# Kernel optimization log

Hardware: AMD Instinct MI355X
Metric: run time of the kernel (lower is better)

The kernel has to match this reference:

```python
import jax, jax.numpy as jnp
import numpy as np

B, N, L, E = 8, 2000, 128, 2048  # batch, nodes, local_size+1, ff_hidden_dim
PENALTY = 10.0


def setup_inputs() -> dict:
    key = jax.random.key(0)
    ks = jax.random.split(key, 8)
    dist = jax.random.uniform(ks[0], (B, N, N), jnp.float32) + 1e-3  # positive distances
    theta = jax.random.normal(ks[1], (B, N, N), jnp.float32)
    ins_feature0 = jax.random.normal(ks[2], (B, N, 1), jnp.float32)
    ins_feature1 = jax.random.normal(ks[3], (B, N, 1), jnp.float32)
    d_in = 2 * L + 2
    W1 = jax.random.normal(ks[4], (d_in, E), jnp.float32) * 0.02
    b1 = jnp.zeros((E,), jnp.float32)
    W2 = jax.random.normal(ks[5], (E, L), jnp.float32) * 0.02
    b2 = jnp.zeros((L,), jnp.float32)
    return {"theta": theta, "dist": dist, "ins_feature0": ins_feature0,
            "ins_feature1": ins_feature1, "W1": W1, "b1": b1, "W2": W2, "b2": b2}


def reference(theta, dist, ins_feature0, ins_feature1, W1, b1, W2, b2):
    k = W2.shape[1]  # local_size (L)
    # smallest-k along last dim, sorted ascending (torch.topk largest=False)
    neg_vals, idx = jax.lax.top_k(-dist, k)          # [B,N,L]
    sorted_dist = -neg_vals
    sorted_dist = sorted_dist / jnp.max(sorted_dist, axis=-1, keepdims=True)
    sorted_theta = jnp.take_along_axis(theta, idx, axis=-1)  # [B,N,L]
    x_in = jnp.concatenate([sorted_dist, sorted_theta, ins_feature0, ins_feature1], axis=-1)  # [B,N,2L+2]
    edge_emb = x_in @ W1 + b1                        # [B,N,E] (no nonlinearity, as in source)
    out = edge_emb @ W2 + b2 - sorted_dist           # [B,N,L]
    b_, n_, _ = dist.shape
    bi = jnp.arange(b_)[:, None, None]
    ni = jnp.arange(n_)[None, :, None]
    out_mat = jnp.full(dist.shape, PENALTY, dist.dtype).at[bi, ni, idx].set(out)
    return out_mat
```

## Files before the change

### kernel.cpp

```cpp
#include <hip/hip_runtime.h>
#include <hip/hip_bf16.h>

#define BN 8
#define NN 2000
#define LL 128
#define EE 2048
#define DIN 258
#define KPAD 264
#define NROWS (BN*NN)
#define PENALTY_V 10.0f
#define CANDCAP 256
#define T0 0.092f
#define SPLITK 16
#define ECHUNK (EE/SPLITK)
#define RPB 4
#define NBINS 256
#define AWORDS 5568

__global__ __launch_bounds__(256) void kA1(const float* __restrict__ W1,
                                           const float* __restrict__ b1,
                                           const float* __restrict__ W2,
                                           float* __restrict__ part) {
    __shared__ float As2[8][64];
    const int t = threadIdx.x;
    const int j = t & 127;
    const int half = t >> 7;
    const int rg = blockIdx.x >> 4;
    const int ks = blockIdx.x & 15;
    const int k0 = rg * 8;
    const int ebase = ks * ECHUNK;
    float acc[4] = {0.f, 0.f, 0.f, 0.f};
    for (int ec = ebase; ec < ebase + ECHUNK; ec += 64) {
        #pragma unroll
        for (int q = 0; q < 2; ++q) {
            int linear = q * 256 + t;
            int r8 = linear >> 6;
            int e  = linear & 63;
            int k  = k0 + r8;
            float v;
            if (k < DIN)       v = W1[k * EE + ec + e];
            else if (k == DIN) v = b1[ec + e];
            else               v = 0.0f;
            As2[r8][e] = v;
        }
        __syncthreads();
        #pragma unroll 8
        for (int e = 0; e < 64; ++e) {
            float w = W2[(ec + e) * LL + j];
            #pragma unroll
            for (int rr = 0; rr < 4; ++rr)
                acc[rr] += As2[half * 4 + rr][e] * w;
        }
        __syncthreads();
    }
    #pragma unroll
    for (int rr = 0; rr < 4; ++rr) {
        int k = k0 + half * 4 + rr;
        part[(size_t)ks * (KPAD * LL) + k * LL + j] = acc[rr];
    }
}

__global__ __launch_bounds__(256) void kA2(const float* __restrict__ part,
                                           const float* __restrict__ b2,
                                           float* __restrict__ Wc,
                                           float* __restrict__ bc) {
    const int i = blockIdx.x * 256 + threadIdx.x;
    float s = 0.f;
    #pragma unroll
    for (int q = 0; q < SPLITK; ++q) s += part[(size_t)q * (KPAD * LL) + i];
    const int k = i >> 7;
    const int j = i & 127;
    if (k == DIN)      { bc[j] = s + b2[j]; Wc[i] = 0.f; }
    else if (k > DIN)  { Wc[i] = 0.f; }
    else               { Wc[i] = s; }
}

__global__ __launch_bounds__(256) void kZ(unsigned int* __restrict__ cursor) {
    int i = blockIdx.x * 256 + threadIdx.x;
    if (i < NROWS) cursor[i] = 0u;
}

__global__ __launch_bounds__(256) void kPA(const float* __restrict__ dist,
                                           unsigned long long* __restrict__ candg,
                                           unsigned int* __restrict__ cursor) {
    const int t = threadIdx.x;
    const int lane = t & 63;
    const int row = blockIdx.x;
    unsigned int v[8];
    unsigned int mask8 = 0u;
    int cnt_l = 0;
    if (t < 250) {
        const uint4* d4 = (const uint4*)(dist + (size_t)row * NN);
        uint4 a = d4[2 * t], b = d4[2 * t + 1];
        v[0] = a.x; v[1] = a.y; v[2] = a.z; v[3] = a.w;
        v[4] = b.x; v[5] = b.y; v[6] = b.z; v[7] = b.w;
        #pragma unroll
        for (int e = 0; e < 8; ++e)
            if (__uint_as_float(v[e]) <= T0) mask8 |= (1u << e);
        cnt_l = __builtin_popcount(mask8);
    }
    int inc = cnt_l;
    #pragma unroll
    for (int d = 1; d < 64; d <<= 1) {
        int o = __shfl_up(inc, d);
        if (lane >= d) inc += o;
    }
    const int excl = inc - cnt_l;
    unsigned int ret = 0u;
    if (lane == 63) ret = atomicAdd(&cursor[row], (unsigned int)inc);
    const unsigned int base = (unsigned int)__shfl((int)ret, 63);
    unsigned int off = base + (unsigned int)excl;
    #pragma unroll
    for (int e = 0; e < 8; ++e) {
        if ((mask8 >> e) & 1u) {
            if (off < (unsigned int)CANDCAP)
                candg[(size_t)row * CANDCAP + off] =
                    ((unsigned long long)v[e] << 32) | (unsigned int)(8 * t + e);
            ++off;
        }
    }
}

__global__ __launch_bounds__(256) void kPB(const float* __restrict__ dist,
                                           const float* __restrict__ theta,
                                           const float* __restrict__ f0,
                                           const float* __restrict__ f1,
                                           const unsigned long long* __restrict__ candg,
                                           const unsigned int* __restrict__ cursor,
                                           const float* __restrict__ Wc,
                                           const float* __restrict__ bc,
                                           float* __restrict__ out) {
    __shared__ __align__(16) unsigned int arena[AWORDS];
    const int t = threadIdx.x;
    const int lane = t & 63;
    const int w = t >> 6;
    const int row = blockIdx.x * RPB + w;

    float* xv = (float*)&arena[4000 + w * 264];
    int* oidx = (int*)&arena[5056 + w * 128];
    const unsigned int cnt = cursor[row];

    if (cnt >= (unsigned int)LL && cnt <= (unsigned int)CANDCAP) {
        unsigned long long* keys = (unsigned long long*)&arena[w * 1000];
        unsigned long long k0v, k1v, k2v, k3v;
        {
            const unsigned long long* cg = candg + (size_t)row * CANDCAP;
            k0v = (lane        < (int)cnt) ? cg[lane]        : ~0ULL;
            k1v = (lane + 64   < (int)cnt) ? cg[lane + 64]   : ~0ULL;
            k2v = (lane + 128  < (int)cnt) ? cg[lane + 128]  : ~0ULL;
            k3v = (lane + 192  < (int)cnt) ? cg[lane + 192]  : ~0ULL;
            keys[lane] = k0v; keys[lane + 64] = k1v;
            keys[lane + 128] = k2v; keys[lane + 192] = k3v;
        }
        float th0 = 0.f, th1 = 0.f, th2 = 0.f, th3 = 0.f;
        if (k0v != ~0ULL) th0 = theta[(size_t)row * NN + (unsigned int)k0v];
        if (k1v != ~0ULL) th1 = theta[(size_t)row * NN + (unsigned int)k1v];
        if (k2v != ~0ULL) th2 = theta[(size_t)row * NN + (unsigned int)k2v];
        if (k3v != ~0ULL) th3 = theta[(size_t)row * NN + (unsigned int)k3v];
        unsigned int r0 = 0, r1 = 0, r2 = 0, r3 = 0;
        for (unsigned int j = 0; j < cnt; ++j) {
            const unsigned long long kj = keys[j];
            r0 += (kj < k0v); r1 += (kj < k1v);
            r2 += (kj < k2v); r3 += (kj < k3v);
        }
        if (k0v != ~0ULL && r0 < (unsigned int)LL) {
            xv[r0] = __uint_as_float((unsigned int)(k0v >> 32));
            xv[LL + r0] = th0; oidx[r0] = (int)(unsigned int)k0v;
        }
        if (k1v != ~0ULL && r1 < (unsigned int)LL) {
            xv[r1] = __uint_as_float((unsigned int)(k1v >> 32));
            xv[LL + r1] = th1; oidx[r1] = (int)(unsigned int)k1v;
        }
        if (k2v != ~0ULL && r2 < (unsigned int)LL) {
            xv[r2] = __uint_as_float((unsigned int)(k2v >> 32));
            xv[LL + r2] = th2; oidx[r2] = (int)(unsigned int)k2v;
        }
        if (k3v != ~0ULL && r3 < (unsigned int)LL) {
            xv[r3] = __uint_as_float((unsigned int)(k3v >> 32));
            xv[LL + r3] = th3; oidx[r3] = (int)(unsigned int)k3v;
        }
    } else {
        unsigned int* hist = &arena[w * 1000];
        unsigned long long* cand = (unsigned long long*)&arena[w * 1000 + 256];
        {
            uint4 z4 = {0u, 0u, 0u, 0u};
            *(uint4*)&hist[lane * 4] = z4;
            unsigned long long f1v = ~0ULL;
            #pragma unroll
            for (int q = 0; q < CANDCAP / 64; ++q) cand[lane + q * 64] = f1v;
        }
        unsigned int v[32];
        const int nv = (lane < 52) ? 32 : 28;
        {
            const uint4* drow4 = (const uint4*)(dist + (size_t)row * NN);
            #pragma unroll
            for (int q = 0; q < 8; ++q) {
                int qi = q * 64 + lane;
                if (qi < NN / 4) {
                    uint4 a = drow4[qi];
                    v[4 * q] = a.x; v[4 * q + 1] = a.y;
                    v[4 * q + 2] = a.z; v[4 * q + 3] = a.w;
                }
            }
        }
        float T = T0;
        unsigned int qm = 0u;
        {
            unsigned int lmax = 0u;
            #pragma unroll
            for (int k = 0; k < 32; ++k) if (k < nv) lmax = max(lmax, v[k]);
            #pragma unroll
            for (int d = 1; d < 64; d <<= 1) lmax = max(lmax, (unsigned int)__shfl_xor((int)lmax, d));
            float lo = 0.0f, hi = __uint_as_float(lmax);
            if (cnt < (unsigned int)LL) lo = T; else hi = T;
            for (int it = 0; it < 32; ++it) {
                T = 0.5f * (lo + hi);
                unsigned int m = 0u;
                #pragma unroll
                for (int k = 0; k < 32; ++k)
                    if (k < nv && __uint_as_float(v[k]) <= T) m |= (1u << k);
                int c = __builtin_popcount(m);
                #pragma unroll
                for (int d = 1; d < 64; d <<= 1) c += __shfl_xor(c, d);
                qm = m;
                if (c >= LL && c <= CANDCAP) break;
                if (c < LL) lo = T; else hi = T;
            }
        }
        const float scale2 = (float)(NBINS - 1) / T;
        #pragma unroll
        for (int k = 0; k < 32; ++k) {
            if ((qm >> k) & 1u) {
                float f = __uint_as_float(v[k]);
                int b = (int)(f * scale2);
                b = b > NBINS - 1 ? NBINS - 1 : b;
                atomicAdd(&hist[b], 1u);
            }
        }
        {
            uint4* h4 = (uint4*)&hist[lane * 4];
            uint4 a0 = *h4;
            unsigned int c[4] = {a0.x, a0.y, a0.z, a0.w};
            unsigned int loc[4], run = 0;
            #pragma unroll
            for (int k = 0; k < 4; ++k) { loc[k] = run; run += c[k]; }
            unsigned int inc = run;
            #pragma unroll
            for (int d = 1; d < 64; d <<= 1) {
                unsigned int o = (unsigned int)__shfl_up((int)inc, d);
                if (lane >= d) inc += o;
            }
            const unsigned int excl = inc - run;
            uint4 s0 = {excl + loc[0], excl + loc[1], excl + loc[2], excl + loc[3]};
            *h4 = s0;
        }
        #pragma unroll
        for (int k = 0; k < 32; ++k) {
            if ((qm >> k) & 1u) {
                unsigned int bits = v[k];
                float f = __uint_as_float(bits);
                int b = (int)(f * scale2);
                b = b > NBINS - 1 ? NBINS - 1 : b;
                unsigned int old = atomicAdd(&hist[b], 0x10000u);
                unsigned int slot = (old & 0xFFFFu) + (old >> 16);
                unsigned int idx = (unsigned int)((k >> 2) * 256 + lane * 4 + (k & 3));
                if (slot < (unsigned int)CANDCAP)
                    cand[slot] = ((unsigned long long)bits << 32) | idx;
            }
        }
        {
            unsigned long long key_s[CANDCAP / 64];
            float th_s[CANDCAP / 64];
            #pragma unroll
            for (int s = 0; s < CANDCAP / 64; ++s) key_s[s] = cand[lane + s * 64];
            #pragma unroll
            for (int s = 0; s < CANDCAP / 64; ++s)
                if (key_s[s] != ~0ULL)
                    th_s[s] = theta[(size_t)row * NN + (unsigned int)key_s[s]];
            #pragma unroll
            for (int s = 0; s < CANDCAP / 64; ++s) {
                unsigned long long key = key_s[s];
                if (key != ~0ULL) {
                    unsigned int bits = (unsigned int)(key >> 32);
                    unsigned int idx  = (unsigned int)key;
                    float f = __uint_as_float(bits);
                    int b = (int)(f * scale2);
                    b = b > NBINS - 1 ? NBINS - 1 : b;
                    unsigned int word = hist[b];
                    unsigned int start = word & 0xFFFFu;
                    unsigned int end = start + (word >> 16);
                    if (end > (unsigned int)CANDCAP) end = (unsigned int)CANDCAP;
                    unsigned int r = start;
                    for (unsigned int j = start; j < end; ++j) r += (cand[j] < key);
                    if (r < (unsigned int)LL) {
                        xv[r] = f;
                        xv[LL + r] = th_s[s];
                        oidx[r] = (int)idx;
                    }
                }
            }
        }
    }

    {
        const float rdm = 1.0f / xv[LL - 1];
        xv[lane] *= rdm;
        xv[lane + 64] *= rdm;
        if (lane == 0) {
            xv[256] = f0[row];
            xv[257] = f1[row];
            #pragma unroll
            for (int z = DIN; z < KPAD; ++z) xv[z] = 0.0f;
        }
    }

    __syncthreads();

    const int j = t & 127;
    const int rp = t >> 7;
    const float* x0 = (const float*)&arena[4000 + (2 * rp) * 264];
    const float* x1 = (const float*)&arena[4000 + (2 * rp + 1) * 264];
    float acc0 = bc[j] - x0[j];
    float acc1 = bc[j] - x1[j];
    #pragma unroll 2
    for (int k = 0; k < KPAD; k += 8) {
        float w0 = Wc[(k + 0) * LL + j];
        float w1 = Wc[(k + 1) * LL + j];
        float w2 = Wc[(k + 2) * LL + j];
        float w3 = Wc[(k + 3) * LL + j];
        float w4 = Wc[(k + 4) * LL + j];
        float w5 = Wc[(k + 5) * LL + j];
        float w6 = Wc[(k + 6) * LL + j];
        float w7 = Wc[(k + 7) * LL + j];
        float4 xa0 = *(const float4*)&x0[k];
        float4 xa1 = *(const float4*)&x0[k + 4];
        float4 xb0 = *(const float4*)&x1[k];
        float4 xb1 = *(const float4*)&x1[k + 4];
        acc0 += xa0.x * w0; acc1 += xb0.x * w0;
        acc0 += xa0.y * w1; acc1 += xb0.y * w1;
        acc0 += xa0.z * w2; acc1 += xb0.z * w2;
        acc0 += xa0.w * w3; acc1 += xb0.w * w3;
        acc0 += xa1.x * w4; acc1 += xb1.x * w4;
        acc0 += xa1.y * w5; acc1 += xb1.y * w5;
        acc0 += xa1.z * w6; acc1 += xb1.z * w6;
        acc0 += xa1.w * w7; acc1 += xb1.w * w7;
    }
    const int oi0 = ((const int*)&arena[5056 + (2 * rp) * 128])[j];
    const int oi1 = ((const int*)&arena[5056 + (2 * rp + 1) * 128])[j];

    float* rowbuf = (float*)arena;
    const float4 pen4 = {PENALTY_V, PENALTY_V, PENALTY_V, PENALTY_V};
    #pragma unroll
    for (int p = 0; p < 2; ++p) {
        __syncthreads();
        for (int i = t; i < 1000; i += 256) ((float4*)rowbuf)[i] = pen4;
        __syncthreads();
        if (rp == p) {
            rowbuf[oi0] = acc0;
            rowbuf[NN + oi1] = acc1;
        }
        __syncthreads();
        float4* o4 = (float4*)(out + ((size_t)blockIdx.x * RPB + 2 * p) * NN);
        for (int i = t; i < 1000; i += 256) o4[i] = ((const float4*)rowbuf)[i];
    }
}

extern "C" void kernel_launch(void* const* d_in, const int* in_sizes, int n_in,
                              void* d_out, int out_size, void* d_ws, size_t ws_size,
                              hipStream_t stream) {
    const float* theta = (const float*)d_in[0];
    const float* dist  = (const float*)d_in[1];
    const float* f0    = (const float*)d_in[2];
    const float* f1    = (const float*)d_in[3];
    const float* W1    = (const float*)d_in[4];
    const float* b1    = (const float*)d_in[5];
    const float* W2    = (const float*)d_in[6];
    const float* b2    = (const float*)d_in[7];
    float* out = (float*)d_out;

    char* ws = (char*)d_ws;
    float* Wc   = (float*)ws;
    float* bc   = (float*)(ws + 135168);
    float* part = (float*)(ws + 135680);
    unsigned long long* candg = (unsigned long long*)(ws + 135680);
    unsigned int* cursor = (unsigned int*)(ws + 135680 + 32768000);

    kA1<<<33 * SPLITK, 256, 0, stream>>>(W1, b1, W2, part);
    kA2<<<(KPAD * LL) / 256, 256, 0, stream>>>(part, b2, Wc, bc);
    kZ<<<(NROWS + 255) / 256, 256, 0, stream>>>(cursor);
    kPA<<<NROWS, 256, 0, stream>>>(dist, candg, cursor);
    kPB<<<NROWS / RPB, 256, 0, stream>>>(dist, theta, f0, f1, candg, cursor, Wc, bc, out);
}
```

Before: 138.0 us.

## Bucket candidates by histogram before ranking and transpose combined weight matrix

In the fast path, candidates are now bucketed into a shared-memory histogram over distance bins, and each key's rank is computed only against keys in its own bucket plus the bucket's prefix offset. This replaces the full O(cnt) comparison loop per key. Separately, the folded weight matrix is stored transposed so each thread reads its weight column with contiguous float4 loads instead of eight strided scalar loads. The transposed layout makes lanes in a wavefront read addresses KPAD apart, which may hurt coalescing compared with the original layout, and the atomics add shared-memory contention.

```diff
diff --git a/kernel.cpp b/kernel.cpp
--- a/kernel.cpp
+++ b/kernel.cpp
@@ -62,7 +62,7 @@
 
 __global__ __launch_bounds__(256) void kA2(const float* __restrict__ part,
                                            const float* __restrict__ b2,
-                                           float* __restrict__ Wc,
+                                           float* __restrict__ WcT,
                                            float* __restrict__ bc) {
     const int i = blockIdx.x * 256 + threadIdx.x;
     float s = 0.f;
@@ -70,9 +70,9 @@
     for (int q = 0; q < SPLITK; ++q) s += part[(size_t)q * (KPAD * LL) + i];
     const int k = i >> 7;
     const int j = i & 127;
-    if (k == DIN)      { bc[j] = s + b2[j]; Wc[i] = 0.f; }
-    else if (k > DIN)  { Wc[i] = 0.f; }
-    else               { Wc[i] = s; }
+    if (k == DIN)      { bc[j] = s + b2[j]; WcT[j * KPAD + k] = 0.f; }
+    else if (k > DIN)  { WcT[j * KPAD + k] = 0.f; }
+    else               { WcT[j * KPAD + k] = s; }
 }
 
 __global__ __launch_bounds__(256) void kZ(unsigned int* __restrict__ cursor) {
@@ -127,7 +127,7 @@
                                            const float* __restrict__ f1,
                                            const unsigned long long* __restrict__ candg,
                                            const unsigned int* __restrict__ cursor,
-                                           const float* __restrict__ Wc,
+                                           const float* __restrict__ WcT,
                                            const float* __restrict__ bc,
                                            float* __restrict__ out) {
     __shared__ __align__(16) unsigned int arena[AWORDS];
@@ -138,50 +138,77 @@
 
     float* xv = (float*)&arena[4000 + w * 264];
     int* oidx = (int*)&arena[5056 + w * 128];
+    unsigned int* hist = &arena[w * 1000];
+    unsigned long long* cand = (unsigned long long*)&arena[w * 1000 + 256];
     const unsigned int cnt = cursor[row];
 
     if (cnt >= (unsigned int)LL && cnt <= (unsigned int)CANDCAP) {
-        unsigned long long* keys = (unsigned long long*)&arena[w * 1000];
-        unsigned long long k0v, k1v, k2v, k3v;
-        {
-            const unsigned long long* cg = candg + (size_t)row * CANDCAP;
-            k0v = (lane        < (int)cnt) ? cg[lane]        : ~0ULL;
-            k1v = (lane + 64   < (int)cnt) ? cg[lane + 64]   : ~0ULL;
-            k2v = (lane + 128  < (int)cnt) ? cg[lane + 128]  : ~0ULL;
-            k3v = (lane + 192  < (int)cnt) ? cg[lane + 192]  : ~0ULL;
-            keys[lane] = k0v; keys[lane + 64] = k1v;
-            keys[lane + 128] = k2v; keys[lane + 192] = k3v;
-        }
-        float th0 = 0.f, th1 = 0.f, th2 = 0.f, th3 = 0.f;
-        if (k0v != ~0ULL) th0 = theta[(size_t)row * NN + (unsigned int)k0v];
-        if (k1v != ~0ULL) th1 = theta[(size_t)row * NN + (unsigned int)k1v];
-        if (k2v != ~0ULL) th2 = theta[(size_t)row * NN + (unsigned int)k2v];
-        if (k3v != ~0ULL) th3 = theta[(size_t)row * NN + (unsigned int)k3v];
-        unsigned int r0 = 0, r1 = 0, r2 = 0, r3 = 0;
-        for (unsigned int j = 0; j < cnt; ++j) {
-            const unsigned long long kj = keys[j];
-            r0 += (kj < k0v); r1 += (kj < k1v);
-            r2 += (kj < k2v); r3 += (kj < k3v);
-        }
-        if (k0v != ~0ULL && r0 < (unsigned int)LL) {
-            xv[r0] = __uint_as_float((unsigned int)(k0v >> 32));
-            xv[LL + r0] = th0; oidx[r0] = (int)(unsigned int)k0v;
-        }
-        if (k1v != ~0ULL && r1 < (unsigned int)LL) {
-            xv[r1] = __uint_as_float((unsigned int)(k1v >> 32));
-            xv[LL + r1] = th1; oidx[r1] = (int)(unsigned int)k1v;
-        }
-        if (k2v != ~0ULL && r2 < (unsigned int)LL) {
-            xv[r2] = __uint_as_float((unsigned int)(k2v >> 32));
-            xv[LL + r2] = th2; oidx[r2] = (int)(unsigned int)k2v;
-        }
-        if (k3v != ~0ULL && r3 < (unsigned int)LL) {
-            xv[r3] = __uint_as_float((unsigned int)(k3v >> 32));
-            xv[LL + r3] = th3; oidx[r3] = (int)(unsigned int)k3v;
+        {
+            uint4 z4 = {0u, 0u, 0u, 0u};
+            *(uint4*)&hist[lane * 4] = z4;
+        }
+        unsigned long long ks[4];
+        float th[4];
+        const unsigned long long* cg = candg + (size_t)row * CANDCAP;
+        #pragma unroll
+        for (int s = 0; s < 4; ++s)
+            ks[s] = ((unsigned int)(lane + s * 64) < cnt) ? cg[lane + s * 64] : ~0ULL;
+        #pragma unroll
+        for (int s = 0; s < 4; ++s)
+            if (ks[s] != ~0ULL)
+                th[s] = theta[(size_t)row * NN + (unsigned int)ks[s]];
+        const float scaleT = (float)(NBINS - 1) / T0;
+        int bk[4];
+        #pragma unroll
+        for (int s = 0; s < 4; ++s) {
+            if (ks[s] != ~0ULL) {
+                float f = __uint_as_float((unsigned int)(ks[s] >> 32));
+                int b = (int)(f * scaleT);
+                bk[s] = b > NBINS - 1 ? NBINS - 1 : b;
+                atomicAdd(&hist[bk[s]], 1u);
+            }
+        }
+        {
+            uint4* h4 = (uint4*)&hist[lane * 4];
+            uint4 a0 = *h4;
+            unsigned int c[4] = {a0.x, a0.y, a0.z, a0.w};
+            unsigned int loc[4], run = 0;
+            #pragma unroll
+            for (int k = 0; k < 4; ++k) { loc[k] = run; run += c[k]; }
+            unsigned int inc = run;
+            #pragma unroll
+            for (int d = 1; d < 64; d <<= 1) {
+                unsigned int o = (unsigned int)__shfl_up((int)inc, d);
+                if (lane >= d) inc += o;
+            }
+            const unsigned int excl = inc - run;
+            uint4 s0 = {excl + loc[0], excl + loc[1], excl + loc[2], excl + loc[3]};
+            *h4 = s0;
+        }
+        #pragma unroll
+        for (int s = 0; s < 4; ++s) {
+            if (ks[s] != ~0ULL) {
+                unsigned int old = atomicAdd(&hist[bk[s]], 0x10000u);
+                unsigned int slot = (old & 0xFFFFu) + (old >> 16);
+                cand[slot] = ks[s];
+            }
+        }
+        #pragma unroll
+        for (int s = 0; s < 4; ++s) {
+            if (ks[s] != ~0ULL) {
+                unsigned int word = hist[bk[s]];
+                unsigned int start = word & 0xFFFFu;
+                unsigned int end = start + (word >> 16);
+                unsigned int r = start;
+                for (unsigned int jj = start; jj < end; ++jj) r += (cand[jj] < ks[s]);
+                if (r < (unsigned int)LL) {
+                    xv[r] = __uint_as_float((unsigned int)(ks[s] >> 32));
+                    xv[LL + r] = th[s];
+                    oidx[r] = (int)(unsigned int)ks[s];
+                }
+            }
         }
     } else {
-        unsigned int* hist = &arena[w * 1000];
-        unsigned long long* cand = (unsigned long long*)&arena[w * 1000 + 256];
         {
             uint4 z4 = {0u, 0u, 0u, 0u};
             *(uint4*)&hist[lane * 4] = z4;
@@ -291,7 +318,7 @@
                     unsigned int end = start + (word >> 16);
                     if (end > (unsigned int)CANDCAP) end = (unsigned int)CANDCAP;
                     unsigned int r = start;
-                    for (unsigned int j = start; j < end; ++j) r += (cand[j] < key);
+                    for (unsigned int jj = start; jj < end; ++jj) r += (cand[jj] < key);
                     if (r < (unsigned int)LL) {
                         xv[r] = f;
                         xv[LL + r] = th_s[s];
@@ -320,30 +347,25 @@
     const int rp = t >> 7;
     const float* x0 = (const float*)&arena[4000 + (2 * rp) * 264];
     const float* x1 = (const float*)&arena[4000 + (2 * rp + 1) * 264];
+    const float* wrow = WcT + (size_t)j * KPAD;
     float acc0 = bc[j] - x0[j];
     float acc1 = bc[j] - x1[j];
     #pragma unroll 2
     for (int k = 0; k < KPAD; k += 8) {
-        float w0 = Wc[(k + 0) * LL + j];
-        float w1 = Wc[(k + 1) * LL + j];
-        float w2 = Wc[(k + 2) * LL + j];
-        float w3 = Wc[(k + 3) * LL + j];
-        float w4 = Wc[(k + 4) * LL + j];
-        float w5 = Wc[(k + 5) * LL + j];
-        float w6 = Wc[(k + 6) * LL + j];
-        float w7 = Wc[(k + 7) * LL + j];
+        float4 wa0 = *(const float4*)&wrow[k];
+        float4 wa1 = *(const float4*)&wrow[k + 4];
         float4 xa0 = *(const float4*)&x0[k];
         float4 xa1 = *(const float4*)&x0[k + 4];
         float4 xb0 = *(const float4*)&x1[k];
         float4 xb1 = *(const float4*)&x1[k + 4];
-        acc0 += xa0.x * w0; acc1 += xb0.x * w0;
-        acc0 += xa0.y * w1; acc1 += xb0.y * w1;
-        acc0 += xa0.z * w2; acc1 += xb0.z * w2;
-        acc0 += xa0.w * w3; acc1 += xb0.w * w3;
-        acc0 += xa1.x * w4; acc1 += xb1.x * w4;
-        acc0 += xa1.y * w5; acc1 += xb1.y * w5;
-        acc0 += xa1.z * w6; acc1 += xb1.z * w6;
-        acc0 += xa1.w * w7; acc1 += xb1.w * w7;
+        acc0 += xa0.x * wa0.x; acc1 += xb0.x * wa0.x;
+        acc0 += xa0.y * wa0.y; acc1 += xb0.y * wa0.y;
+        acc0 += xa0.z * wa0.z; acc1 += xb0.z * wa0.z;
+        acc0 += xa0.w * wa0.w; acc1 += xb0.w * wa0.w;
+        acc0 += xa1.x * wa1.x; acc1 += xb1.x * wa1.x;
+        acc0 += xa1.y * wa1.y; acc1 += xb1.y * wa1.y;
+        acc0 += xa1.z * wa1.z; acc1 += xb1.z * wa1.z;
+        acc0 += xa1.w * wa1.w; acc1 += xb1.w * wa1.w;
     }
     const int oi0 = ((const int*)&arena[5056 + (2 * rp) * 128])[j];
     const int oi1 = ((const int*)&arena[5056 + (2 * rp + 1) * 128])[j];
@@ -379,15 +401,15 @@
     float* out = (float*)d_out;
 
     char* ws = (char*)d_ws;
-    float* Wc   = (float*)ws;
+    float* WcT  = (float*)ws;
     float* bc   = (float*)(ws + 135168);
     float* part = (float*)(ws + 135680);
     unsigned long long* candg = (unsigned long long*)(ws + 135680);
     unsigned int* cursor = (unsigned int*)(ws + 135680 + 32768000);
 
     kA1<<<33 * SPLITK, 256, 0, stream>>>(W1, b1, W2, part);
-    kA2<<<(KPAD * LL) / 256, 256, 0, stream>>>(part, b2, Wc, bc);
+    kA2<<<(KPAD * LL) / 256, 256, 0, stream>>>(part, b2, WcT, bc);
     kZ<<<(NROWS + 255) / 256, 256, 0, stream>>>(cursor);
     kPA<<<NROWS, 256, 0, stream>>>(dist, candg, cursor);
-    kPB<<<NROWS / RPB, 256, 0, stream>>>(dist, theta, f0, f1, candg, cursor, Wc, bc, out);
-}
+    kPB<<<NROWS / RPB, 256, 0, stream>>>(dist, theta, f0, f1, candg, cursor, WcT, bc, out);
+}
```

After: 182.3 us. 1.32x slower.
